# Kernel optimization log

Measured on AMD Instinct MI355X. Metric: run time of the kernel, lower is better.

The kernel has to match this reference:

```python
import jax, jax.numpy as jnp
import numpy as np

EPS = 1e-6
N_NFT, N_TRADER, D = 16384, 8192, 8
NNZ = 2_000_000


def setup_inputs() -> dict:
    key = jax.random.key(0)
    k1, k2, k3, k4, k5, k6, k7 = jax.random.split(key, 7)
    return {
        "latent_z": jax.random.normal(k1, (N_NFT, D), dtype=jnp.float32),
        "latent_q": jax.random.normal(k2, (N_TRADER, D), dtype=jnp.float32),
        "gamma": jax.random.normal(k3, (N_NFT,), dtype=jnp.float32),
        "delta": jax.random.normal(k4, (N_TRADER,), dtype=jnp.float32),
        "weights": jax.random.uniform(k5, (NNZ,), dtype=jnp.float32),
        "sparse_i": jax.random.randint(k6, (NNZ,), 0, N_NFT, dtype=jnp.int64) if jax.config.jax_enable_x64 else jax.random.randint(k6, (NNZ,), 0, N_NFT, dtype=jnp.int32),
        "sparse_j": jax.random.randint(k7, (NNZ,), 0, N_TRADER, dtype=jnp.int32),
    }


def reference(latent_z, latent_q, gamma, delta, weights, sparse_i, sparse_j):
    # --- dense normalizer: exp(gamma)^T @ exp(-(cdist(z+eps, q)+eps)) @ exp(delta)
    z = latent_z + EPS  # torch.cdist(self.latent_z + 1e-6, self.latent_q)
    zn = jnp.sum(z * z, axis=-1)                     # [N]
    qn = jnp.sum(latent_q * latent_q, axis=-1)       # [M]
    d2 = zn[:, None] + qn[None, :] - 2.0 * (z @ latent_q.T)  # [N, M]
    dist = jnp.sqrt(jnp.maximum(d2, 0.0))
    mat = jnp.exp(-(dist + EPS))                     # [N, M]
    z_pdist1 = jnp.exp(gamma) @ mat @ jnp.exp(delta)  # scalar

    # --- sparse Poisson log-likelihood term over observed edges
    diff = latent_z[sparse_i] - latent_q[sparse_j] + EPS  # [nnz, D]
    zqdist = -jnp.sqrt(jnp.sum(diff * diff, axis=-1))     # [nnz]
    z_pdist2 = jnp.sum(weights * (gamma[sparse_i] + delta[sparse_j] + zqdist))

    return z_pdist2 - z_pdist1
```

## Files before the change

### kernel.cpp

```cpp
#include <hip/hip_runtime.h>

#define EPSF 1e-6f
#define L2E  1.44269504088896340736f

using bf16x8 = __attribute__((ext_vector_type(8))) short;
using f32x16 = __attribute__((ext_vector_type(16))) float;

constexpr int NT   = 256;
constexpr int JC   = 512;
constexpr int NJC  = 8192 / JC;
constexpr int RPAN = 128;
constexpr int NRP  = 16384 / RPAN;
constexpr int NB   = NRP * NJC;
constexpr int JT   = JC / 32;
constexpr int RSTR = 16;

__device__ __forceinline__ short f2bf(float f) {
    union { float f; unsigned u; } c{f};
    return (short)((c.u + 0x7fffu + ((c.u >> 16) & 1u)) >> 16);
}
__device__ __forceinline__ float bf2f(short s) {
    union { unsigned u; float f; } c{((unsigned)(unsigned short)s) << 16};
    return c.f;
}

__device__ __forceinline__ float block_reduce_sum(float v) {
#pragma unroll
    for (int off = 32; off > 0; off >>= 1) v += __shfl_down(v, off, 64);
    __shared__ float parts[4];
    const int t = threadIdx.x;
    if ((t & 63) == 0) parts[t >> 6] = v;
    __syncthreads();
    float r = 0.f;
    if (t == 0) r = parts[0] + parts[1] + parts[2] + parts[3];
    return r;
}

__device__ __forceinline__ bf16x8 make_afrag(const float* __restrict__ z,
                                             int row, int half) {
    const float4 a = *(const float4*)(z + (size_t)row * 8);
    const float4 b = *(const float4*)(z + (size_t)row * 8 + 4);
    const float h[8] = {L2E * (a.x + EPSF), L2E * (a.y + EPSF),
                        L2E * (a.z + EPSF), L2E * (a.w + EPSF),
                        L2E * (b.x + EPSF), L2E * (b.y + EPSF),
                        L2E * (b.z + EPSF), L2E * (b.w + EPSF)};
    short s[8];
    float zn = 0.f;
#pragma unroll
    for (int d = 0; d < 8; ++d) {
        s[d] = f2bf(h[d]);
        const float r = bf2f(s[d]);
        zn = fmaf(r, r, zn);
    }
    bf16x8 f;
    if (half == 0) {
        f[0] = s[0]; f[1] = s[1]; f[2] = s[2]; f[3] = s[3];
        f[4] = s[4]; f[5] = s[5]; f[6] = s[6]; f[7] = s[7];
    } else {
        f[0] = f2bf(zn); f[1] = (short)0x3F80;
        f[2] = 0; f[3] = 0; f[4] = 0; f[5] = 0; f[6] = 0; f[7] = 0;
    }
    return f;
}

__global__ __launch_bounds__(NT) void fused_kernel(
    const float* __restrict__ z, const float* __restrict__ q,
    const float* __restrict__ gamma, const float* __restrict__ delta,
    const float* __restrict__ w, const int* __restrict__ si,
    const int* __restrict__ sj, int nnz, float* __restrict__ partial)
{
    __shared__ short sqb[JC * RSTR];
    __shared__ float sld[JC];
    __shared__ float seg[RPAN];

    const int t      = threadIdx.x;
    const int id     = blockIdx.x;
    const int jc     = id & (NJC - 1);
    const int rpan   = id >> 4;
    const int c0     = jc * JC;
    const int r0base = rpan * RPAN;

    if (t < RPAN) seg[t] = __expf(gamma[r0base + t]);
#pragma unroll
    for (int c = t; c < JC; c += NT) {
        const int C = c0 + c;
        const float4 a = *(const float4*)(q + (size_t)C * 8);
        const float4 b = *(const float4*)(q + (size_t)C * 8 + 4);
        const float h[8] = {L2E * a.x, L2E * a.y, L2E * a.z, L2E * a.w,
                            L2E * b.x, L2E * b.y, L2E * b.z, L2E * b.w};
        float qn = 0.f;
#pragma unroll
        for (int d = 0; d < 8; ++d) {
            const short s = f2bf(h[d]);
            const float r = bf2f(s);
            qn = fmaf(r, r, qn);
            sqb[c * RSTR + d] = f2bf(-2.f * r);
        }
        sqb[c * RSTR + 8] = (short)0x3F80;
        sqb[c * RSTR + 9] = f2bf(qn);
#pragma unroll
        for (int d = 10; d < 16; ++d) sqb[c * RSTR + d] = 0;
        sld[c] = L2E * (delta[C] - EPSF);
    }

    const int wv   = t >> 6;
    const int lane = t & 63;
    const int li   = lane & 31;
    const int half = lane >> 5;
    const bf16x8 afrag = make_afrag(z, r0base + wv * 32 + li, half);

    float sacc = 0.f;
    for (int k = id * NT + t; k < nnz; k += NB * NT) {
        const int i = si[k];
        const int j = sj[k];
        const float4 a = *(const float4*)(z + (size_t)i * 8);
        const float4 b = *(const float4*)(z + (size_t)i * 8 + 4);
        const float4 c = *(const float4*)(q + (size_t)j * 8);
        const float4 d = *(const float4*)(q + (size_t)j * 8 + 4);
        const float d0 = a.x - c.x + EPSF, d1 = a.y - c.y + EPSF;
        const float d2 = a.z - c.z + EPSF, d3 = a.w - c.w + EPSF;
        const float d4 = b.x - d.x + EPSF, d5 = b.y - d.y + EPSF;
        const float d6 = b.z - d.z + EPSF, d7 = b.w - d.w + EPSF;
        float s2 = d0 * d0;
        s2 = fmaf(d1, d1, s2); s2 = fmaf(d2, d2, s2); s2 = fmaf(d3, d3, s2);
        s2 = fmaf(d4, d4, s2); s2 = fmaf(d5, d5, s2); s2 = fmaf(d6, d6, s2);
        s2 = fmaf(d7, d7, s2);
        sacc = fmaf(w[k], gamma[i] + delta[j] - __builtin_amdgcn_sqrtf(s2), sacc);
    }
    __syncthreads();

    float acc[16];
#pragma unroll
    for (int r = 0; r < 16; ++r) acc[r] = 0.f;

#pragma unroll
    for (int jt = 0; jt < JT; ++jt) {
        const bf16x8 bfrag = *(const bf16x8*)&sqb[(jt * 32 + li) * RSTR + half * 8];
        const float  ld_l  = sld[jt * 32 + li];
        f32x16 s = __builtin_amdgcn_mfma_f32_32x32x16_bf16(
            afrag, bfrag, (f32x16)(0.f), 0, 0, 0);
#pragma unroll
        for (int r = 0; r < 16; ++r) {
            const float st = __builtin_amdgcn_sqrtf(__builtin_fabsf(s[r]));
            acc[r] += __builtin_amdgcn_exp2f(ld_l - st);
        }
    }

    float vv = 0.f;
#pragma unroll
    for (int r4 = 0; r4 < 4; ++r4)
#pragma unroll
        for (int r0 = 0; r0 < 4; ++r0)
            vv = fmaf(seg[wv * 32 + half * 4 + r0 + 8 * r4], acc[r4 * 4 + r0], vv);

    const float v = block_reduce_sum(sacc - vv);
    if (t == 0) partial[id] = v;
}

__global__ __launch_bounds__(256) void reduce_kernel(
    const float* __restrict__ partial, int n, float* __restrict__ out)
{
    float v = 0.f;
    for (int k = threadIdx.x; k < n; k += 256) v += partial[k];
    v = block_reduce_sum(v);
    if (threadIdx.x == 0) out[0] = v;
}

extern "C" void kernel_launch(void* const* d_in, const int* in_sizes, int n_in,
                              void* d_out, int out_size, void* d_ws, size_t ws_size,
                              hipStream_t stream) {
    const float* z     = (const float*)d_in[0];
    const float* q     = (const float*)d_in[1];
    const float* gamma = (const float*)d_in[2];
    const float* delta = (const float*)d_in[3];
    const float* w     = (const float*)d_in[4];
    const int*   si    = (const int*)d_in[5];
    const int*   sj    = (const int*)d_in[6];
    const int    nnz   = in_sizes[4];

    float* out = (float*)d_out;
    float* ws  = (float*)d_ws;

    fused_kernel<<<NB, NT, 0, stream>>>(z, q, gamma, delta, w, si, sj, nnz, ws);
    reduce_kernel<<<1, 256, 0, stream>>>(ws, NB, out);
}
```

Baseline: 48.03 us.

## Split B-fragment LDS layout, factor exp(delta) out, run MFMA before sparse loop

The q fragment table in shared memory is split into two contiguous 16-byte halves per column, replacing the padded 16-short stride and the scalar stores with vector stores. The -2 scaling moves to the z fragment. exp(delta) is precomputed per column and applied with an fma after exp2(-dist), which drops a subtract inside the inner loop. The dense MFMA phase now runs before the sparse gather loop, so the sparse loop's memory latency is no longer in front of the barrier.

After: 88.04 us. 1.83x slower.

```diff
diff --git a/kernel.cpp b/kernel.cpp
--- a/kernel.cpp
+++ b/kernel.cpp
@@ -13,7 +13,6 @@
 constexpr int NRP  = 16384 / RPAN;
 constexpr int NB   = NRP * NJC;
 constexpr int JT   = JC / 32;
-constexpr int RSTR = 16;
 
 __device__ __forceinline__ short f2bf(float f) {
     union { float f; unsigned u; } c{f};
@@ -44,19 +43,16 @@
                         L2E * (a.z + EPSF), L2E * (a.w + EPSF),
                         L2E * (b.x + EPSF), L2E * (b.y + EPSF),
                         L2E * (b.z + EPSF), L2E * (b.w + EPSF)};
-    short s[8];
+    bf16x8 f;
     float zn = 0.f;
 #pragma unroll
     for (int d = 0; d < 8; ++d) {
-        s[d] = f2bf(h[d]);
-        const float r = bf2f(s[d]);
+        const short s = f2bf(h[d]);
+        const float r = bf2f(s);
         zn = fmaf(r, r, zn);
+        f[d] = f2bf(-2.f * r);
     }
-    bf16x8 f;
-    if (half == 0) {
-        f[0] = s[0]; f[1] = s[1]; f[2] = s[2]; f[3] = s[3];
-        f[4] = s[4]; f[5] = s[5]; f[6] = s[6]; f[7] = s[7];
-    } else {
+    if (half != 0) {
         f[0] = f2bf(zn); f[1] = (short)0x3F80;
         f[2] = 0; f[3] = 0; f[4] = 0; f[5] = 0; f[6] = 0; f[7] = 0;
     }
@@ -69,18 +65,19 @@
     const float* __restrict__ w, const int* __restrict__ si,
     const int* __restrict__ sj, int nnz, float* __restrict__ partial)
 {
-    __shared__ short sqb[JC * RSTR];
-    __shared__ float sld[JC];
+    __shared__ __align__(16) short sqb[1024 * 8];
+    __shared__ float sed[JC];
     __shared__ float seg[RPAN];
 
-    const int t      = threadIdx.x;
-    const int id     = blockIdx.x;
-    const int jc     = id & (NJC - 1);
-    const int rpan   = id >> 4;
-    const int c0     = jc * JC;
-    const int r0base = rpan * RPAN;
+    const int t    = threadIdx.x;
+    const int id   = blockIdx.x;
+    const int jc   = id & (NJC - 1);
+    const int rpan = id >> 4;
+    const int c0   = jc * JC;
+    const int r0   = rpan * RPAN;
 
-    if (t < RPAN) seg[t] = __expf(gamma[r0base + t]);
+    if (t < RPAN) seg[t] = __expf(gamma[r0 + t]);
+
 #pragma unroll
     for (int c = t; c < JC; c += NT) {
         const int C = c0 + c;
@@ -88,26 +85,58 @@
         const float4 b = *(const float4*)(q + (size_t)C * 8 + 4);
         const float h[8] = {L2E * a.x, L2E * a.y, L2E * a.z, L2E * a.w,
                             L2E * b.x, L2E * b.y, L2E * b.z, L2E * b.w};
+        bf16x8 g0;
         float qn = 0.f;
 #pragma unroll
         for (int d = 0; d < 8; ++d) {
             const short s = f2bf(h[d]);
             const float r = bf2f(s);
             qn = fmaf(r, r, qn);
-            sqb[c * RSTR + d] = f2bf(-2.f * r);
+            g0[d] = s;
         }
-        sqb[c * RSTR + 8] = (short)0x3F80;
-        sqb[c * RSTR + 9] = f2bf(qn);
-#pragma unroll
-        for (int d = 10; d < 16; ++d) sqb[c * RSTR + d] = 0;
-        sld[c] = L2E * (delta[C] - EPSF);
+        *(bf16x8*)&sqb[c * 8] = g0;
+        bf16x8 g1;
+        g1[0] = (short)0x3F80;
+        g1[1] = f2bf(qn);
+        g1[2] = 0; g1[3] = 0; g1[4] = 0; g1[5] = 0; g1[6] = 0; g1[7] = 0;
+        *(bf16x8*)&sqb[(512 + c) * 8] = g1;
+        sed[c] = __expf(delta[C] - EPSF);
     }
 
     const int wv   = t >> 6;
     const int lane = t & 63;
     const int li   = lane & 31;
     const int half = lane >> 5;
-    const bf16x8 afrag = make_afrag(z, r0base + wv * 32 + li, half);
+    const bf16x8 afrag = make_afrag(z, r0 + wv * 32 + li, half);
+
+    __syncthreads();
+
+    const short* bbase = &sqb[(half * 512 + li) * 8];
+    const float* edp   = &sed[li];
+
+    float acc[16];
+#pragma unroll
+    for (int r = 0; r < 16; ++r) acc[r] = 0.f;
+
+#pragma unroll
+    for (int jt = 0; jt < JT; ++jt) {
+        const bf16x8 bfrag = *(const bf16x8*)(bbase + jt * 32 * 8);
+        const float  ed_l  = edp[jt * 32];
+        f32x16 s = __builtin_amdgcn_mfma_f32_32x32x16_bf16(
+            afrag, bfrag, (f32x16)(0.f), 0, 0, 0);
+#pragma unroll
+        for (int r = 0; r < 16; ++r) {
+            const float st = __builtin_amdgcn_sqrtf(__builtin_fabsf(s[r]));
+            acc[r] = fmaf(ed_l, __builtin_amdgcn_exp2f(-st), acc[r]);
+        }
+    }
+
+    float vv = 0.f;
+#pragma unroll
+    for (int r4 = 0; r4 < 4; ++r4)
+#pragma unroll
+        for (int rr = 0; rr < 4; ++rr)
+            vv = fmaf(seg[wv * 32 + half * 4 + rr + 8 * r4], acc[r4 * 4 + rr], vv);
 
     float sacc = 0.f;
     for (int k = id * NT + t; k < nnz; k += NB * NT) {
@@ -127,31 +156,6 @@
         s2 = fmaf(d7, d7, s2);
         sacc = fmaf(w[k], gamma[i] + delta[j] - __builtin_amdgcn_sqrtf(s2), sacc);
     }
-    __syncthreads();
-
-    float acc[16];
-#pragma unroll
-    for (int r = 0; r < 16; ++r) acc[r] = 0.f;
-
-#pragma unroll
-    for (int jt = 0; jt < JT; ++jt) {
-        const bf16x8 bfrag = *(const bf16x8*)&sqb[(jt * 32 + li) * RSTR + half * 8];
-        const float  ld_l  = sld[jt * 32 + li];
-        f32x16 s = __builtin_amdgcn_mfma_f32_32x32x16_bf16(
-            afrag, bfrag, (f32x16)(0.f), 0, 0, 0);
-#pragma unroll
-        for (int r = 0; r < 16; ++r) {
-            const float st = __builtin_amdgcn_sqrtf(__builtin_fabsf(s[r]));
-            acc[r] += __builtin_amdgcn_exp2f(ld_l - st);
-        }
-    }
-
-    float vv = 0.f;
-#pragma unroll
-    for (int r4 = 0; r4 < 4; ++r4)
-#pragma unroll
-        for (int r0 = 0; r0 < 4; ++r0)
-            vv = fmaf(seg[wv * 32 + half * 4 + r0 + 8 * r4], acc[r4 * 4 + r0], vv);
 
     const float v = block_reduce_sum(sacc - vv);
     if (t == 0) partial[id] = v;
```
